# Optimization experiments

Hardware: AMD Instinct MI355X
Metric: run time of the kernel (lower is better)

Reference implementation:

```python
import jax, jax.numpy as jnp
import numpy as np

B, CI, CO, H, W, K = 4, 128, 128, 128, 128, 3
KK = K * K
PAD = 1  # padding=1, stride=1, dilation=1
BN_EPS = 1e-3


def setup_inputs() -> dict:
    key = jax.random.key(0)
    ks = jax.random.split(key, 5)
    x = jax.random.normal(ks[0], (B, CI, H, W), jnp.float32)
    # offset conv: 2*K*K output channels, small init so sampled offsets are moderate
    w_off = jax.random.normal(ks[1], (2 * KK, CI, K, K), jnp.float32) * 0.01
    b_off = jnp.zeros((2 * KK,), jnp.float32)
    # deformable conv weight (DeformConv2d has no bias)
    w_dcn = jax.random.normal(ks[2], (CO, CI, K, K), jnp.float32) * (1.0 / np.sqrt(CI * KK))
    gamma = jax.random.uniform(ks[3], (CO,), jnp.float32, minval=0.5, maxval=1.5)
    beta = jax.random.normal(ks[4], (CO,), jnp.float32) * 0.1
    return {"x": x, "w_off": w_off, "b_off": b_off, "w_dcn": w_dcn,
            "gamma": gamma, "beta": beta}


def _deform_block(x, w_off, b_off, w_dcn, gamma, beta):
    Bn, Ci, Hn, Wn = x.shape
    dt = x.dtype

    # --- offset conv (standard 3x3 conv, same padding) ---
    offset = jax.lax.conv_general_dilated(
        x, w_off, window_strides=(1, 1), padding=[(PAD, PAD), (PAD, PAD)],
        dimension_numbers=("NCHW", "OIHW", "NCHW")) + b_off[None, :, None, None]
    off = offset.reshape(Bn, KK, 2, Hn, Wn)
    dy, dx = off[:, :, 0], off[:, :, 1]  # [B, KK, H, W]

    # --- sampling coordinates: base grid + kernel tap + learned offset ---
    ky, kx = jnp.meshgrid(jnp.arange(K), jnp.arange(K), indexing="ij")
    ky = ky.reshape(KK).astype(dt)
    kx = kx.reshape(KK).astype(dt)
    ys = (jnp.arange(Hn, dtype=dt)[None, None, :, None] - PAD
          + ky[None, :, None, None]) + dy                      # [B, KK, H, W]
    xs = (jnp.arange(Wn, dtype=dt)[None, None, None, :] - PAD
          + kx[None, :, None, None]) + dx                      # [B, KK, H, W]

    y0 = jnp.floor(ys)
    x0 = jnp.floor(xs)
    wy = ys - y0  # bilinear weights
    wx = xs - x0

    x_flat = x.reshape(Bn, Ci, Hn * Wn)

    def gather(yi, xi):
        # per-corner zero-padding boundary handling (matches mmcv deform_conv)
        valid = ((yi >= 0) & (yi < Hn) & (xi >= 0) & (xi < Wn)).astype(dt)
        yc = jnp.clip(yi, 0, Hn - 1).astype(jnp.int32)
        xc = jnp.clip(xi, 0, Wn - 1).astype(jnp.int32)
        idx = (yc * Wn + xc).reshape(Bn, -1)                   # [B, KK*H*W]
        v = jax.vmap(lambda f, i: f[:, i])(x_flat, idx)        # [B, Ci, KK*H*W]
        return v.reshape(Bn, Ci, KK, Hn, Wn) * valid.reshape(Bn, 1, KK, Hn, Wn)

    sampled = (gather(y0, x0) * ((1 - wy) * (1 - wx))[:, None]
               + gather(y0, x0 + 1) * ((1 - wy) * wx)[:, None]
               + gather(y0 + 1, x0) * (wy * (1 - wx))[:, None]
               + gather(y0 + 1, x0 + 1) * (wy * wx)[:, None])  # [B, Ci, KK, H, W]

    out = jnp.einsum("bckhw,ock->bohw", sampled, w_dcn.reshape(CO, Ci, KK))

    # --- BatchNorm (training-mode batch stats, biased var) + ReLU ---
    mean = out.mean(axis=(0, 2, 3))
    var = out.var(axis=(0, 2, 3))
    norm = (out - mean[None, :, None, None]) * jax.lax.rsqrt(var + BN_EPS)[None, :, None, None]
    return jax.nn.relu(norm * gamma[None, :, None, None] + beta[None, :, None, None])


def reference(x, w_off, b_off, w_dcn, gamma, beta):
    return _deform_block(x, w_off, b_off, w_dcn, gamma, beta)
```

## Files before the change

### kernel.cpp

```cpp
#include <hip/hip_runtime.h>
#include <hip/hip_bf16.h>

#define NB 4
#define CI 128
#define CO 128
#define HH 128
#define WW 128
#define HW 16384
#define KK 9

typedef __attribute__((ext_vector_type(4))) float f32x4;
typedef __attribute__((ext_vector_type(4))) unsigned int u32x4;
typedef __attribute__((ext_vector_type(8))) short bf16x8;

static __device__ __forceinline__ unsigned short f2bf(float v) {
  __hip_bfloat16 h = __float2bfloat16(v);
  return *reinterpret_cast<const unsigned short*>(&h);
}
static __device__ __forceinline__ unsigned int pk2(float lo, float hi) {
  return (unsigned int)f2bf(lo) | ((unsigned int)f2bf(hi) << 16);
}
static __device__ __forceinline__ float bflo(unsigned int u) {
  return __uint_as_float(u << 16);
}
static __device__ __forceinline__ float bfhi(unsigned int u) {
  return __uint_as_float(u & 0xFFFF0000u);
}

__global__ __launch_bounds__(256) void k_xpose(const float* __restrict__ x,
                                               unsigned short* __restrict__ xT) {
  __shared__ float tile[128][65];
  const int bid = blockIdx.x;
  const int b = bid >> 8;
  const int h = (bid >> 1) & 127;
  const int w0 = (bid & 1) * 64;
  const int t = threadIdx.x;
  const int lw = t & 63;
  const float* xp = x + (size_t)b * CI * HW + h * WW + w0;
#pragma unroll
  for (int k = 0; k < 32; ++k) {
    int ci = (t >> 6) * 32 + k;
    tile[ci][lw] = xp[(size_t)ci * HW + lw];
  }
  __syncthreads();
  unsigned short* op = xT + ((size_t)(b * 128 + h) * 128 + w0) * 128;
  const int ci2 = (t & 63) * 2;
  const int wg = t >> 6;
#pragma unroll
  for (int k = 0; k < 16; ++k) {
    int w = wg * 16 + k;
    unsigned int p = (unsigned int)f2bf(tile[ci2][w]) | ((unsigned int)f2bf(tile[ci2 + 1][w]) << 16);
    *(unsigned int*)(op + (size_t)w * 128 + ci2) = p;
  }
}

__global__ __launch_bounds__(256) void k_wprep3(const float* __restrict__ w,
                                                unsigned short* __restrict__ wT3) {
  int i = blockIdx.x * 256 + threadIdx.x;
  if (i >= CO * CI * KK) return;
  int e = i & 7;
  int colc = (i >> 3) & 15;
  int c = (i >> 7) & 15;
  int nf = (i >> 11) & 7;
  int tap = i >> 14;
  int co = nf * 16 + colc;
  int ci = c * 8 + e;
  wT3[i] = f2bf(w[((size_t)(co * 128 + ci)) * 9 + tap]);
}

__global__ __launch_bounds__(256) void k_wprep2(const float* __restrict__ w,
                                                unsigned short* __restrict__ wT2) {
  int i = blockIdx.x * 256 + threadIdx.x;
  if (i >= 36864) return;
  int e = i & 7;
  int colc = (i >> 3) & 15;
  int c = (i >> 7) & 15;
  int nf = (i >> 11) & 1;
  int tap = i >> 12;
  int oc = nf * 16 + colc;
  unsigned short v = 0;
  if (oc < 18) v = f2bf(w[((size_t)(oc * 128 + c * 8 + e)) * 9 + tap]);
  wT2[i] = v;
}

__global__ __launch_bounds__(256, 2) void k_main(
    const unsigned short* __restrict__ xT, const unsigned short* __restrict__ wT3,
    const unsigned short* __restrict__ wT2, const float* __restrict__ b_off,
    float* __restrict__ outp, float* __restrict__ stats) {
  __shared__ __align__(16) unsigned char xstage[288 * 256];
  __shared__ float off_f[4 * 288];

  const int bid0 = blockIdx.x;
  const int bid = (bid0 & 7) * 128 + (bid0 >> 3);
  const int b = bid >> 8;
  const int rem = bid & 255;
  const int h0 = (rem >> 3) * 4;
  const int w0 = (rem & 7) * 16;
  const int t = threadIdx.x;
  const int l = t & 63;
  const int wv = t >> 6;
  const int colc = l & 15;
  const int kg = l >> 4;
  const int h = h0 + wv;

  const unsigned short* xb = xT + (size_t)b * HW * 128;

  {
    const int base_h = h0 - 4, base_w = w0 - 4;
    const int c = t & 15;
    const int tp = t >> 4;
#pragma unroll
    for (int j = 0; j < 18; ++j) {
      int pix = j * 16 + tp;
      int r = pix / 24, cc = pix - r * 24;
      int gh = base_h + r, gw = base_w + cc;
      u32x4 v = (u32x4){0u, 0u, 0u, 0u};
      if (((unsigned)gh < 128u) && ((unsigned)gw < 128u))
        v = *(const u32x4*)(xb + ((size_t)(gh * 128 + gw)) * 128 + c * 8);
      *(u32x4*)(xstage + pix * 256 + ((c ^ (pix & 15)) << 4)) = v;
    }
  }
  __syncthreads();

  f32x4 oacc0 = (f32x4){0.f, 0.f, 0.f, 0.f};
  f32x4 oacc1 = (f32x4){0.f, 0.f, 0.f, 0.f};
#pragma unroll 1
  for (int tap = 0; tap < KK; ++tap) {
    int ty = tap / 3, tx = tap - ty * 3;
    int pixo = (wv + ty + 3) * 24 + (colc + tx + 3);
    const int pb = pixo * 256, ps = pixo & 15;
#pragma unroll
    for (int ks = 0; ks < 4; ++ks) {
      int c = (ks << 2) | kg;
      u32x4 raw = *(const u32x4*)(xstage + pb + ((c ^ ps) << 4));
      bf16x8 afr = __builtin_bit_cast(bf16x8, raw);
      bf16x8 bf0 = *(const bf16x8*)(wT2 + (((size_t)(tap * 2 + 0) * 16 + c) * 16 + colc) * 8);
      bf16x8 bf1 = *(const bf16x8*)(wT2 + (((size_t)(tap * 2 + 1) * 16 + c) * 16 + colc) * 8);
      oacc0 = __builtin_amdgcn_mfma_f32_16x16x32_bf16(afr, bf0, oacc0, 0, 0, 0);
      oacc1 = __builtin_amdgcn_mfma_f32_16x16x32_bf16(afr, bf1, oacc1, 0, 0, 0);
    }
  }
  {
    float b0 = b_off[colc];
#pragma unroll
    for (int r = 0; r < 4; ++r) off_f[wv * 288 + colc * 16 + kg * 4 + r] = oacc0[r] + b0;
    if (colc < 2) {
      float b1 = b_off[16 + colc];
#pragma unroll
      for (int r = 0; r < 4; ++r) off_f[wv * 288 + (16 + colc) * 16 + kg * 4 + r] = oacc1[r] + b1;
    }
  }

  f32x4 acc[8];
#pragma unroll
  for (int nf = 0; nf < 8; ++nf) acc[nf] = (f32x4){0.f, 0.f, 0.f, 0.f};

#pragma unroll 1
  for (int tap = 0; tap < KK; ++tap) {
    int ty = tap / 3, tx = tap - ty * 3;
    float dy = off_f[wv * 288 + (2 * tap) * 16 + colc];
    float dx = off_f[wv * 288 + (2 * tap + 1) * 16 + colc];
    float ys = (float)(h - 1 + ty) + dy;
    float xs = (float)(w0 + colc - 1 + tx) + dx;
    float y0f = floorf(ys), x0f = floorf(xs);
    float fy = ys - y0f, fx = xs - x0f;
    int iy0 = (int)y0f, ix0 = (int)x0f;
    float fy0 = 1.f - fy, fx0 = 1.f - fx;
    float w00 = fy0 * fx0, w01 = fy0 * fx, w10 = fy * fx0, w11 = fy * fx;
    int rs = min(max(iy0 - (h0 - 4), 0), 10);
    int cs = min(max(ix0 - (w0 - 4), 0), 22);
    int p00 = rs * 24 + cs;
    int p01 = p00 + 1, p10 = p00 + 24, p11 = p00 + 25;
    const int b00 = p00 * 256, s00 = p00 & 15;
    const int b01 = p01 * 256, s01 = p01 & 15;
    const int b10 = p10 * 256, s10 = p10 & 15;
    const int b11 = p11 * 256, s11 = p11 & 15;
#pragma unroll
    for (int ks = 0; ks < 4; ++ks) {
      int c = (ks << 2) | kg;
      u32x4 r00 = *(const u32x4*)(xstage + b00 + ((c ^ s00) << 4));
      u32x4 r01 = *(const u32x4*)(xstage + b01 + ((c ^ s01) << 4));
      u32x4 r10 = *(const u32x4*)(xstage + b10 + ((c ^ s10) << 4));
      u32x4 r11 = *(const u32x4*)(xstage + b11 + ((c ^ s11) << 4));
      bf16x8 bfr[8];
#pragma unroll
      for (int nf = 0; nf < 8; ++nf)
        bfr[nf] = *(const bf16x8*)(wT3 + (((size_t)(tap * 8 + nf) * 16 + c) * 16 + colc) * 8);
      u32x4 pkv;
#pragma unroll
      for (int j = 0; j < 4; ++j) {
        float vlo = w00 * bflo(r00[j]) + w01 * bflo(r01[j]) + w10 * bflo(r10[j]) +
                    w11 * bflo(r11[j]);
        float vhi = w00 * bfhi(r00[j]) + w01 * bfhi(r01[j]) + w10 * bfhi(r10[j]) +
                    w11 * bfhi(r11[j]);
        pkv[j] = pk2(vlo, vhi);
      }
      bf16x8 afr = __builtin_bit_cast(bf16x8, pkv);
#pragma unroll
      for (int nf = 0; nf < 8; ++nf)
        acc[nf] = __builtin_amdgcn_mfma_f32_16x16x32_bf16(afr, bfr[nf], acc[nf], 0, 0, 0);
    }
  }

  const size_t ob = (size_t)b * CO * HW;
#pragma unroll
  for (int nf = 0; nf < 8; ++nf) {
    int co = nf * 16 + colc;
    *(f32x4*)&outp[ob + (size_t)co * HW + h * WW + w0 + kg * 4] = acc[nf];
  }
  float* myred = off_f + wv * 288;
#pragma unroll
  for (int nf = 0; nf < 8; ++nf) {
    float s = acc[nf][0] + acc[nf][1] + acc[nf][2] + acc[nf][3];
    float sq = acc[nf][0] * acc[nf][0] + acc[nf][1] * acc[nf][1] + acc[nf][2] * acc[nf][2] +
               acc[nf][3] * acc[nf][3];
    s += __shfl_xor(s, 16);
    s += __shfl_xor(s, 32);
    sq += __shfl_xor(sq, 16);
    sq += __shfl_xor(sq, 32);
    if (kg == 0) {
      int co = nf * 16 + colc;
      myred[co] = s;
      myred[144 + co] = sq;
    }
  }
  __syncthreads();
  if (t < 128) {
    float s = off_f[t] + off_f[288 + t] + off_f[576 + t] + off_f[864 + t];
    atomicAdd(&stats[t], s);
  } else if (t < 256) {
    int c2 = t - 128;
    float q = off_f[144 + c2] + off_f[288 + 144 + c2] + off_f[576 + 144 + c2] +
              off_f[864 + 144 + c2];
    atomicAdd(&stats[CO + c2], q);
  }
}

__global__ void k_stats(const float* __restrict__ stats, const float* __restrict__ gamma,
                        const float* __restrict__ beta, float* __restrict__ sc) {
  int co = threadIdx.x;
  const float inv = 1.f / 65536.f;
  float mean = stats[co] * inv;
  float var = stats[CO + co] * inv - mean * mean;
  float scale = rsqrtf(var + 1e-3f) * gamma[co];
  sc[co] = scale;
  sc[CO + co] = beta[co] - mean * scale;
}

__global__ __launch_bounds__(256) void k_bn(float* __restrict__ outp,
                                            const float* __restrict__ sc) {
  int i = blockIdx.x * 256 + threadIdx.x;
  f32x4 v = ((const f32x4*)outp)[i];
  int co = (i >> 12) & 127;
  float scale = sc[co], shift = sc[CO + co];
#pragma unroll
  for (int j = 0; j < 4; ++j) {
    float y = v[j] * scale + shift;
    v[j] = y > 0.f ? y : 0.f;
  }
  ((f32x4*)outp)[i] = v;
}

extern "C" void kernel_launch(void* const* d_in, const int* in_sizes, int n_in,
                              void* d_out, int out_size, void* d_ws, size_t ws_size,
                              hipStream_t stream) {
  const float* x = (const float*)d_in[0];
  const float* w_off = (const float*)d_in[1];
  const float* b_off = (const float*)d_in[2];
  const float* w_dcn = (const float*)d_in[3];
  const float* gamma = (const float*)d_in[4];
  const float* beta = (const float*)d_in[5];
  float* out = (float*)d_out;
  char* ws = (char*)d_ws;

  unsigned short* wT3 = (unsigned short*)(ws);
  unsigned short* wT2 = (unsigned short*)(ws + 294912);
  unsigned short* xT = (unsigned short*)(ws + 368640);
  float* stats = (float*)(ws + 17145856);
  float* sc = (float*)(ws + 17146880);

  hipMemsetAsync(stats, 0, 1024, stream);
  k_wprep3<<<576, 256, 0, stream>>>(w_dcn, wT3);
  k_wprep2<<<144, 256, 0, stream>>>(w_off, wT2);
  k_xpose<<<1024, 256, 0, stream>>>(x, xT);
  k_main<<<1024, 256, 0, stream>>>(xT, wT3, wT2, b_off, out, stats);
  k_stats<<<1, 128, 0, stream>>>(stats, gamma, beta, sc);
  k_bn<<<8192, 256, 0, stream>>>(out, sc);
}
```

Measured before the change: 249.1 us.

## Move BN statistics out of main kernel into separate reduction pass

Removes the per-block shuffle/LDS reduction and atomicAdd of BN sums from the main deformable conv kernel, along with the memset and single-block stats kernel. A new per-channel kernel re-reads the conv output to compute sum and sum-of-squares, then derives scale/shift. The main kernel also gets explicit waves-per-EU attributes and a partially unrolled staging loop to ease register pressure. The cost is an extra full read of the 32MB output buffer, traded for a lighter main-kernel epilogue and no atomic contention.

```diff
diff --git a/kernel.cpp b/kernel.cpp
--- a/kernel.cpp
+++ b/kernel.cpp
@@ -83,10 +83,10 @@
   wT2[i] = v;
 }
 
-__global__ __launch_bounds__(256, 2) void k_main(
-    const unsigned short* __restrict__ xT, const unsigned short* __restrict__ wT3,
-    const unsigned short* __restrict__ wT2, const float* __restrict__ b_off,
-    float* __restrict__ outp, float* __restrict__ stats) {
+__global__ __attribute__((amdgpu_flat_work_group_size(256, 256), amdgpu_waves_per_eu(2, 2)))
+void k_main(const unsigned short* __restrict__ xT, const unsigned short* __restrict__ wT3,
+            const unsigned short* __restrict__ wT2, const float* __restrict__ b_off,
+            float* __restrict__ outp) {
   __shared__ __align__(16) unsigned char xstage[288 * 256];
   __shared__ float off_f[4 * 288];
 
@@ -109,7 +109,7 @@
     const int base_h = h0 - 4, base_w = w0 - 4;
     const int c = t & 15;
     const int tp = t >> 4;
-#pragma unroll
+#pragma unroll 6
     for (int j = 0; j < 18; ++j) {
       int pix = j * 16 + tp;
       int r = pix / 24, cc = pix - r * 24;
@@ -208,43 +208,49 @@
     int co = nf * 16 + colc;
     *(f32x4*)&outp[ob + (size_t)co * HW + h * WW + w0 + kg * 4] = acc[nf];
   }
-  float* myred = off_f + wv * 288;
-#pragma unroll
-  for (int nf = 0; nf < 8; ++nf) {
-    float s = acc[nf][0] + acc[nf][1] + acc[nf][2] + acc[nf][3];
-    float sq = acc[nf][0] * acc[nf][0] + acc[nf][1] * acc[nf][1] + acc[nf][2] * acc[nf][2] +
-               acc[nf][3] * acc[nf][3];
-    s += __shfl_xor(s, 16);
-    s += __shfl_xor(s, 32);
-    sq += __shfl_xor(sq, 16);
-    sq += __shfl_xor(sq, 32);
-    if (kg == 0) {
-      int co = nf * 16 + colc;
-      myred[co] = s;
-      myred[144 + co] = sq;
-    }
+}
+
+__global__ __launch_bounds__(256) void k_redstats(const float* __restrict__ outp,
+                                                  const float* __restrict__ gamma,
+                                                  const float* __restrict__ beta,
+                                                  float* __restrict__ sc) {
+  __shared__ float red[8];
+  const int co = blockIdx.x;
+  const int t = threadIdx.x;
+  float s = 0.f, sq = 0.f;
+#pragma unroll 1
+  for (int b = 0; b < 4; ++b) {
+    const f32x4* q = (const f32x4*)(outp + ((size_t)b * CO + co) * HW);
+#pragma unroll 4
+    for (int i = t; i < HW / 4; i += 256) {
+      f32x4 v = q[i];
+#pragma unroll
+      for (int j = 0; j < 4; ++j) {
+        s += v[j];
+        sq += v[j] * v[j];
+      }
+    }
+  }
+#pragma unroll
+  for (int d = 1; d < 64; d <<= 1) {
+    s += __shfl_xor(s, d);
+    sq += __shfl_xor(sq, d);
+  }
+  if ((t & 63) == 0) {
+    red[(t >> 6) * 2] = s;
+    red[(t >> 6) * 2 + 1] = sq;
   }
   __syncthreads();
-  if (t < 128) {
-    float s = off_f[t] + off_f[288 + t] + off_f[576 + t] + off_f[864 + t];
-    atomicAdd(&stats[t], s);
-  } else if (t < 256) {
-    int c2 = t - 128;
-    float q = off_f[144 + c2] + off_f[288 + 144 + c2] + off_f[576 + 144 + c2] +
-              off_f[864 + 144 + c2];
-    atomicAdd(&stats[CO + c2], q);
-  }
-}
-
-__global__ void k_stats(const float* __restrict__ stats, const float* __restrict__ gamma,
-                        const float* __restrict__ beta, float* __restrict__ sc) {
-  int co = threadIdx.x;
-  const float inv = 1.f / 65536.f;
-  float mean = stats[co] * inv;
-  float var = stats[CO + co] * inv - mean * mean;
-  float scale = rsqrtf(var + 1e-3f) * gamma[co];
-  sc[co] = scale;
-  sc[CO + co] = beta[co] - mean * scale;
+  if (t == 0) {
+    float S = red[0] + red[2] + red[4] + red[6];
+    float Q = red[1] + red[3] + red[5] + red[7];
+    const float inv = 1.f / 65536.f;
+    float mean = S * inv;
+    float var = Q * inv - mean * mean;
+    float scale = rsqrtf(var + 1e-3f) * gamma[co];
+    sc[co] = scale;
+    sc[CO + co] = beta[co] - mean * scale;
+  }
 }
 
 __global__ __launch_bounds__(256) void k_bn(float* __restrict__ outp,
@@ -276,14 +282,12 @@
   unsigned short* wT3 = (unsigned short*)(ws);
   unsigned short* wT2 = (unsigned short*)(ws + 294912);
   unsigned short* xT = (unsigned short*)(ws + 368640);
-  float* stats = (float*)(ws + 17145856);
-  float* sc = (float*)(ws + 17146880);
-
-  hipMemsetAsync(stats, 0, 1024, stream);
+  float* sc = (float*)(ws + 17145856);
+
   k_wprep3<<<576, 256, 0, stream>>>(w_dcn, wT3);
   k_wprep2<<<144, 256, 0, stream>>>(w_off, wT2);
   k_xpose<<<1024, 256, 0, stream>>>(x, xT);
-  k_main<<<1024, 256, 0, stream>>>(xT, wT3, wT2, b_off, out, stats);
-  k_stats<<<1, 128, 0, stream>>>(stats, gamma, beta, sc);
+  k_main<<<1024, 256, 0, stream>>>(xT, wT3, wT2, b_off, out);
+  k_redstats<<<128, 256, 0, stream>>>(out, gamma, beta, sc);
   k_bn<<<8192, 256, 0, stream>>>(out, sc);
 }
```

Measured after the change: 240.5 us. 1.04x faster.
